# Optimization experiments

Hardware: AMD Instinct MI355X
Metric: run time of the kernel (lower is better)

## Reference

```python
import jax, jax.numpy as jnp
import numpy as np

NQ = 8          # n_qubits (attention and ffn)
DIM = 2 ** NQ   # state-vector dimension
EPS = 1e-5      # nn.LayerNorm default eps


def _layernorm(x, g, b):
    m = jnp.mean(x, axis=-1, keepdims=True)
    v = jnp.mean((x - m) ** 2, axis=-1, keepdims=True)
    return (x - m) * jax.lax.rsqrt(v + EPS) * g + b


def _attn_quantum(tok, theta):
    """Batched 8-qubit state-vector sim: RX(tok_i)+RX(theta_i) per wire, CNOT ring, <Z_i>.
    tok: [N, 8] -> returns [N, 8]."""
    N = tok.shape[0]
    half = 0.5 * (tok + theta)  # RX(a)RX(b) = RX(a+b) on same wire
    # per-wire amplitude RX(a)|0> = (cos(a/2), -i sin(a/2))
    re = jnp.stack([jnp.cos(half), jnp.zeros_like(half)], axis=-1)
    im = jnp.stack([jnp.zeros_like(half), -jnp.sin(half)], axis=-1)
    amp = jax.lax.complex(re, im)  # [N, 8, 2]
    # build product state with wire 0 as the leading qubit axis: [N, 2, ..., 2]
    state = amp[:, 0, :]
    for w in range(1, NQ):
        state = state[..., None] * amp[:, w, :].reshape((N,) + (1,) * w + (2,))
    # CNOT ring: (0,1),(1,2),...,(6,7),(7,0)
    pairs = [(i, i + 1) for i in range(NQ - 1)] + [(NQ - 1, 0)]
    for c, t in pairs:
        flipped = jnp.flip(state, axis=t + 1)
        mask = jnp.arange(2).reshape((1,) * (c + 1) + (2,) + (1,) * (NQ - 1 - c))
        state = jnp.where(mask == 1, flipped, state)
    probs = (state.real ** 2 + state.imag ** 2).reshape(N, DIM)
    # <Z_w> = sum_k probs[k] * (1 - 2*bit_w(k)); wire 0 is most significant bit
    bits = (jnp.arange(DIM)[None, :] >> (NQ - 1 - jnp.arange(NQ)[:, None])) & 1
    signs = (1.0 - 2.0 * bits).astype(probs.dtype)  # [8, 256]
    return probs @ signs.T


def _ffn_quantum(tok, phi):
    """Product state per wire: RY(phi_i) RX(tok_i) |0>, then <Z_i>. tok: [..., 8]."""
    ct, st = jnp.cos(0.5 * tok), jnp.sin(0.5 * tok)
    cp, sp = jnp.cos(0.5 * phi), jnp.sin(0.5 * phi)
    # v0 = cp*ct + i*sp*st ; v1 = sp*ct - i*cp*st ; z = |v0|^2 - |v1|^2
    return (cp * ct) ** 2 + (sp * st) ** 2 - (sp * ct) ** 2 - (cp * st) ** 2


def setup_inputs() -> dict:
    key = jax.random.key(0)
    ks = jax.random.split(key, 8)
    B, S, E, F = 32, 2048, 8, 2048
    x = jax.random.normal(ks[0], (B, S, E), dtype=jnp.float32)
    theta = jax.random.uniform(ks[1], (NQ,), dtype=jnp.float32, minval=-np.pi, maxval=np.pi)
    phi = jax.random.uniform(ks[2], (NQ,), dtype=jnp.float32, minval=-np.pi, maxval=np.pi)
    W1 = jax.random.normal(ks[3], (F, NQ), dtype=jnp.float32) / np.sqrt(NQ)
    b1 = jax.random.normal(ks[4], (F,), dtype=jnp.float32) * 0.01
    W2 = jax.random.normal(ks[5], (E, F), dtype=jnp.float32) / np.sqrt(F)
    b2 = jax.random.normal(ks[6], (E,), dtype=jnp.float32) * 0.01
    gamma1 = jnp.ones((E,), dtype=jnp.float32)
    beta1 = jnp.zeros((E,), dtype=jnp.float32)
    gamma2 = jnp.ones((E,), dtype=jnp.float32)
    beta2 = jnp.zeros((E,), dtype=jnp.float32)
    return {"x": x, "theta": theta, "phi": phi, "W1": W1, "b1": b1, "W2": W2,
            "b2": b2, "gamma1": gamma1, "beta1": beta1, "gamma2": gamma2, "beta2": beta2}


def reference(x, theta, phi, W1, b1, W2, b2, gamma1, beta1, gamma2, beta2):
    B, S, E = x.shape
    attn = _attn_quantum(x.reshape(B * S, E), theta).reshape(B, S, E)
    h = _layernorm(x + attn, gamma1, beta1)            # dropout is identity (eval)
    z = _ffn_quantum(h, phi)                            # [B, S, 8]
    f = jax.nn.relu(z @ W1.T + b1) @ W2.T + b2          # linear1 -> relu -> linear2
    return _layernorm(h + f, gamma2, beta2)
```

## Files before the change

### kernel.cpp

```cpp
#include <hip/hip_runtime.h>
#include <math.h>

#define NQ 8
#define FDIM 2048
#define EPSV 1e-5f

typedef __attribute__((ext_vector_type(8))) short short8v;
typedef __attribute__((ext_vector_type(16))) float f32x16;

__device__ __forceinline__ unsigned pk_bf16(float lo, float hi) {
    unsigned r;
    asm("v_cvt_pk_bf16_f32 %0, %1, %2" : "=v"(r) : "v"(lo), "v"(hi));
    return r;
}

__device__ __forceinline__ short8v pack4(unsigned a, unsigned b, unsigned c, unsigned d) {
    uint4 w; w.x = a; w.y = b; w.z = c; w.w = d;
    return __builtin_bit_cast(short8v, w);
}

#define MFMA32 __builtin_amdgcn_mfma_f32_32x32x16_bf16

#define RP(C, d0, d1)                                                   \
  { const f32x16 m_ = __builtin_elementwise_max(C, zeroC);              \
    d0 = pack4(pk_bf16(m_[0],  m_[1]),  pk_bf16(m_[2],  m_[3]),         \
               pk_bf16(m_[4],  m_[5]),  pk_bf16(m_[6],  m_[7]));        \
    d1 = pack4(pk_bf16(m_[8],  m_[9]),  pk_bf16(m_[10], m_[11]),        \
               pk_bf16(m_[12], m_[13]), pk_bf16(m_[14], m_[15])); }

#define ITER(AUSE, ALOAD, B0USE, B1USE, C2IDX)                          \
  {                                                                     \
    short8v p00, p01, p10, p11;                                         \
    RP(C1_0, p00, p01); RP(C1_1, p10, p11);                             \
    C1_0 = MFMA32(AUSE, b1S0, zeroC, 0, 0, 0);                          \
    C1_1 = MFMA32(AUSE, b1S1, zeroC, 0, 0, 0);                          \
    acc0 = MFMA32(p00, B0USE, acc0, 0, 0, 0);                           \
    acc1 = MFMA32(p10, B0USE, acc1, 0, 0, 0);                           \
    acc0 = MFMA32(p01, B1USE, acc0, 0, 0, 0);                           \
    acc1 = MFMA32(p11, B1USE, acc1, 0, 0, 0);                           \
    short8v p20, p21, p30, p31;                                         \
    RP(C1_2, p20, p21); RP(C1_3, p30, p31);                             \
    C1_2 = MFMA32(AUSE, b1S2, zeroC, 0, 0, 0);                          \
    C1_3 = MFMA32(AUSE, b1S3, zeroC, 0, 0, 0);                          \
    acc2 = MFMA32(p20, B0USE, acc2, 0, 0, 0);                           \
    acc3 = MFMA32(p30, B0USE, acc3, 0, 0, 0);                           \
    acc2 = MFMA32(p21, B1USE, acc2, 0, 0, 0);                           \
    acc3 = MFMA32(p31, B1USE, acc3, 0, 0, 0);                           \
    ALOAD = *reinterpret_cast<const short8v*>(W1p + (C2IDX) * 512);     \
    B0USE = *reinterpret_cast<const short8v*>(W2p + (C2IDX) * 32);      \
    B1USE = *reinterpret_cast<const short8v*>(W2p + (C2IDX) * 32 + 16); \
  }

__launch_bounds__(512, 2)
__global__ void qtb_kernel(const float* __restrict__ x,
                           const float* __restrict__ theta,
                           const float* __restrict__ phi,
                           const float* __restrict__ W1,
                           const float* __restrict__ b1,
                           const float* __restrict__ W2,
                           const float* __restrict__ b2,
                           const float* __restrict__ g1,
                           const float* __restrict__ be1,
                           const float* __restrict__ g2,
                           const float* __restrict__ be2,
                           float* __restrict__ out)
{
    __shared__ short W1f[64 * 512];
    __shared__ short W2s[8 * 2056];
    __shared__ float park[8][1024];
    __shared__ float hLds[256 * 8];

    const int tid  = threadIdx.x;
    const int lane = tid & 63;
    const int wid  = tid >> 6;
    const int g    = wid & 1;
    const int q    = wid >> 1;
    const int hi2  = lane >> 5;
    const int il   = lane & 31;
    const int tbase = blockIdx.x * 256 + g * 128;

    const float4 xA0 = reinterpret_cast<const float4*>(x + (size_t)(tbase + lane) * NQ)[0];
    const float4 xA1 = reinterpret_cast<const float4*>(x + (size_t)(tbase + lane) * NQ)[1];
    const float4 xB0 = reinterpret_cast<const float4*>(x + (size_t)(tbase + 64 + lane) * NQ)[0];
    const float4 xB1 = reinterpret_cast<const float4*>(x + (size_t)(tbase + 64 + lane) * NQ)[1];

    float4 w1lo[4], w1hi[4]; float bk4[4];
#pragma unroll
    for (int it = 0; it < 4; ++it) {
        const int k = tid + it * 512;
        w1lo[it] = *reinterpret_cast<const float4*>(W1 + (size_t)k * NQ);
        w1hi[it] = *reinterpret_cast<const float4*>(W1 + (size_t)k * NQ + 4);
        bk4[it]  = b1[k];
    }
    float4 w2v[8];
#pragma unroll
    for (int it = 0; it < 8; ++it) {
        const int idx = tid + it * 512;
        const int i = idx >> 9, kq = idx & 511;
        w2v[it] = *reinterpret_cast<const float4*>(W2 + (size_t)i * FDIM + kq * 4);
    }

    float h[2][8];
    unsigned zpkt[2][4];
#pragma unroll
    for (int tt = 0; tt < 2; ++tt) {
        const float4 x0 = tt ? xB0 : xA0;
        const float4 x1 = tt ? xB1 : xA1;
        const float xv[8] = {x0.x, x0.y, x0.z, x0.w, x1.x, x1.y, x1.z, x1.w};

        float c[8];
#pragma unroll
        for (int j = 0; j < 8; ++j) c[j] = __cosf(xv[j] + theta[j]);
        float attn[8];
        attn[0] = ((c[1] * c[2]) * (c[3] * c[4])) * ((c[5] * c[6]) * c[7]);
        {
            float p = c[0];
#pragma unroll
            for (int j = 1; j < 8; ++j) { p *= c[j]; attn[j] = p; }
        }
        float s[8];
#pragma unroll
        for (int j = 0; j < 8; ++j) s[j] = xv[j] + attn[j];
        float mean = 0.f;
#pragma unroll
        for (int j = 0; j < 8; ++j) mean += s[j];
        mean *= 0.125f;
        float var = 0.f;
#pragma unroll
        for (int j = 0; j < 8; ++j) { float d = s[j] - mean; var = fmaf(d, d, var); }
        var *= 0.125f;
        const float rs = rsqrtf(var + EPSV);
#pragma unroll
        for (int j = 0; j < 8; ++j) h[tt][j] = (s[j] - mean) * rs * g1[j] + be1[j];

        float zv[8];
#pragma unroll
        for (int j = 0; j < 8; ++j) zv[j] = __cosf(phi[j]) * __cosf(h[tt][j]);
#pragma unroll
        for (int p = 0; p < 4; ++p) zpkt[tt][p] = pk_bf16(zv[2 * p], zv[2 * p + 1]);
    }

    if (q == 0) {
        float4* hp0 = reinterpret_cast<float4*>(&hLds[(g * 128 + lane) * 8]);
        hp0[0] = make_float4(h[0][0], h[0][1], h[0][2], h[0][3]);
        hp0[1] = make_float4(h[0][4], h[0][5], h[0][6], h[0][7]);
        float4* hp1 = reinterpret_cast<float4*>(&hLds[(g * 128 + 64 + lane) * 8]);
        hp1[0] = make_float4(h[1][0], h[1][1], h[1][2], h[1][3]);
        hp1[1] = make_float4(h[1][4], h[1][5], h[1][6], h[1][7]);
    }

    unsigned zs[2][2][4];
#pragma unroll
    for (int tt = 0; tt < 2; ++tt)
#pragma unroll
        for (int p = 0; p < 4; ++p) {
            zs[tt][0][p] = (unsigned)__shfl((int)zpkt[tt][p], il);
            zs[tt][1][p] = (unsigned)__shfl((int)zpkt[tt][p], 32 + il);
        }
    const unsigned biasv = 0x00003f80u;
    const short8v b1S0 = pack4(hi2 ? zs[0][0][2] : zs[0][0][0],
                               hi2 ? zs[0][0][3] : zs[0][0][1],
                               hi2 ? 0u : biasv, 0u);
    const short8v b1S1 = pack4(hi2 ? zs[0][1][2] : zs[0][1][0],
                               hi2 ? zs[0][1][3] : zs[0][1][1],
                               hi2 ? 0u : biasv, 0u);
    const short8v b1S2 = pack4(hi2 ? zs[1][0][2] : zs[1][0][0],
                               hi2 ? zs[1][0][3] : zs[1][0][1],
                               hi2 ? 0u : biasv, 0u);
    const short8v b1S3 = pack4(hi2 ? zs[1][1][2] : zs[1][1][0],
                               hi2 ? zs[1][1][3] : zs[1][1][1],
                               hi2 ? 0u : biasv, 0u);

#pragma unroll
    for (int it = 0; it < 4; ++it) {
        const int k = tid + it * 512;
        uint4 d0, d1;
        d0.x = pk_bf16(w1lo[it].x, w1lo[it].y); d0.y = pk_bf16(w1lo[it].z, w1lo[it].w);
        d0.z = pk_bf16(bk4[it], 0.f);           d0.w = 0u;
        d1.x = pk_bf16(w1hi[it].x, w1hi[it].y); d1.y = pk_bf16(w1hi[it].z, w1hi[it].w);
        d1.z = 0u;                              d1.w = 0u;
        *reinterpret_cast<uint4*>(&W1f[(k >> 5) * 512 + (k & 31) * 8])        = d0;
        *reinterpret_cast<uint4*>(&W1f[(k >> 5) * 512 + ((k & 31) + 32) * 8]) = d1;
    }
#pragma unroll
    for (int it = 0; it < 8; ++it) {
        const int idx = tid + it * 512;
        const int i = idx >> 9, kq = idx & 511;
        const int k0 = kq * 4;
        const int quad = (k0 >> 2) & 3;
        const int posq = (0x3120 >> (quad * 4)) & 0xF;
        const int dcol = (k0 & ~15) | (posq * 4);
        uint2 pkw; pkw.x = pk_bf16(w2v[it].x, w2v[it].y); pkw.y = pk_bf16(w2v[it].z, w2v[it].w);
        *reinterpret_cast<uint2*>(&W2s[i * 2056 + dcol]) = pkw;
    }
    __syncthreads();

    f32x16 zeroC;
#pragma unroll
    for (int e = 0; e < 16; ++e) zeroC[e] = 0.f;
    f32x16 acc0 = zeroC, acc1 = zeroC, acc2 = zeroC, acc3 = zeroC;

    const int ir = il & 7;
    const short* W1p = &W1f[(q * 16) * 512 + lane * 8];
    const short* W2p = &W2s[ir * 2056 + (q * 16) * 32 + hi2 * 8];

    short8v A1a = *reinterpret_cast<const short8v*>(W1p);
    short8v B0a = *reinterpret_cast<const short8v*>(W2p);
    short8v B1a = *reinterpret_cast<const short8v*>(W2p + 16);
    f32x16 C1_0 = MFMA32(A1a, b1S0, zeroC, 0, 0, 0);
    f32x16 C1_1 = MFMA32(A1a, b1S1, zeroC, 0, 0, 0);
    f32x16 C1_2 = MFMA32(A1a, b1S2, zeroC, 0, 0, 0);
    f32x16 C1_3 = MFMA32(A1a, b1S3, zeroC, 0, 0, 0);
    short8v A1b = *reinterpret_cast<const short8v*>(W1p + 512);
    short8v B0b = *reinterpret_cast<const short8v*>(W2p + 32);
    short8v B1b = *reinterpret_cast<const short8v*>(W2p + 32 + 16);

#pragma unroll
    for (int t = 0; t < 16; t += 2) {
        ITER(A1b, A1a, B0a, B1a, (t + 2) & 15);
        ITER(A1a, A1b, B0b, B1b, (t + 3) & 15);
    }

    if (il < 8) {
        float* fb = &park[wid][0];
#pragma unroll
        for (int r = 0; r < 16; ++r) {
            const int trow = (r & 3) + 8 * (r >> 2) + 4 * hi2;
            fb[trow * 8 + il]         = acc0[r];
            fb[(32 + trow) * 8 + il]  = acc1[r];
            fb[(64 + trow) * 8 + il]  = acc2[r];
            fb[(96 + trow) * 8 + il]  = acc3[r];
        }
    }
    __syncthreads();

    if (q == 0) {
#pragma unroll
        for (int tt = 0; tt < 2; ++tt) {
            const int tloc = tt * 64 + lane;
            float fv[8] = {0.f, 0.f, 0.f, 0.f, 0.f, 0.f, 0.f, 0.f};
#pragma unroll
            for (int qq = 0; qq < 4; ++qq) {
                const float* pb = &park[qq * 2 + g][tloc * 8];
                const float4 f0 = *reinterpret_cast<const float4*>(pb);
                const float4 f1 = *reinterpret_cast<const float4*>(pb + 4);
                fv[0] += f0.x; fv[1] += f0.y; fv[2] += f0.z; fv[3] += f0.w;
                fv[4] += f1.x; fv[5] += f1.y; fv[6] += f1.z; fv[7] += f1.w;
            }

            const float4 h0 = reinterpret_cast<const float4*>(&hLds[(g * 128 + tloc) * 8])[0];
            const float4 h1 = reinterpret_cast<const float4*>(&hLds[(g * 128 + tloc) * 8])[1];
            const float hv[8] = {h0.x, h0.y, h0.z, h0.w, h1.x, h1.y, h1.z, h1.w};

            float y[8];
#pragma unroll
            for (int j = 0; j < 8; ++j) y[j] = hv[j] + fv[j] + b2[j];
            float mean2 = 0.f;
#pragma unroll
            for (int j = 0; j < 8; ++j) mean2 += y[j];
            mean2 *= 0.125f;
            float var2 = 0.f;
#pragma unroll
            for (int j = 0; j < 8; ++j) { float d = y[j] - mean2; var2 = fmaf(d, d, var2); }
            var2 *= 0.125f;
            const float rs2 = rsqrtf(var2 + EPSV);

            float o[8];
#pragma unroll
            for (int j = 0; j < 8; ++j) o[j] = (y[j] - mean2) * rs2 * g2[j] + be2[j];

            const int token = blockIdx.x * 256 + g * 128 + tloc;
            float4* op = reinterpret_cast<float4*>(out + (size_t)token * NQ);
            op[0] = make_float4(o[0], o[1], o[2], o[3]);
            op[1] = make_float4(o[4], o[5], o[6], o[7]);
        }
    }
}

extern "C" void kernel_launch(void* const* d_in, const int* in_sizes, int n_in,
                              void* d_out, int out_size, void* d_ws, size_t ws_size,
                              hipStream_t stream) {
    const float* x     = (const float*)d_in[0];
    const float* theta = (const float*)d_in[1];
    const float* phi   = (const float*)d_in[2];
    const float* W1    = (const float*)d_in[3];
    const float* b1    = (const float*)d_in[4];
    const float* W2    = (const float*)d_in[5];
    const float* b2    = (const float*)d_in[6];
    const float* g1    = (const float*)d_in[7];
    const float* be1   = (const float*)d_in[8];
    const float* g2    = (const float*)d_in[9];
    const float* be2   = (const float*)d_in[10];
    float* out = (float*)d_out;

    const int ntok = in_sizes[0] / NQ;
    const int grid = ntok / 256;

    qtb_kernel<<<grid, 512, 0, stream>>>(x, theta, phi, W1, b1, W2, b2,
                                         g1, be1, g2, be2, out);
}
```

Before: 20.56 us.

## Specialize warps: half compute token prologue, half stage weights into LDS

Before, all 8 waves redundantly computed attention, layernorm and z for their token group, and each also loaded a slice of W1/W2. Now waves 0-3 each compute one token per lane once, writing packed z and h to LDS. Waves 4-7 meanwhile load and convert all of W1 and W2 into LDS. The MFMA operands are then read from the zLds buffer instead of built with cross-lane shuffles, and the final layernorm is spread over four waves instead of two. This removes duplicated transcendental work and lets weight staging overlap the prologue, at the cost of more LDS and higher register use in the weight-loading waves.

```diff
diff --git a/kernel.cpp b/kernel.cpp
--- a/kernel.cpp
+++ b/kernel.cpp
@@ -67,8 +67,9 @@
 {
     __shared__ short W1f[64 * 512];
     __shared__ short W2s[8 * 2056];
-    __shared__ float park[8][1024];
+    __shared__ float parkF[8][1024];
     __shared__ float hLds[256 * 8];
+    __shared__ unsigned zLds[256][6];
 
     const int tid  = threadIdx.x;
     const int lane = tid & 63;
@@ -77,35 +78,12 @@
     const int q    = wid >> 1;
     const int hi2  = lane >> 5;
     const int il   = lane & 31;
-    const int tbase = blockIdx.x * 256 + g * 128;
-
-    const float4 xA0 = reinterpret_cast<const float4*>(x + (size_t)(tbase + lane) * NQ)[0];
-    const float4 xA1 = reinterpret_cast<const float4*>(x + (size_t)(tbase + lane) * NQ)[1];
-    const float4 xB0 = reinterpret_cast<const float4*>(x + (size_t)(tbase + 64 + lane) * NQ)[0];
-    const float4 xB1 = reinterpret_cast<const float4*>(x + (size_t)(tbase + 64 + lane) * NQ)[1];
-
-    float4 w1lo[4], w1hi[4]; float bk4[4];
-#pragma unroll
-    for (int it = 0; it < 4; ++it) {
-        const int k = tid + it * 512;
-        w1lo[it] = *reinterpret_cast<const float4*>(W1 + (size_t)k * NQ);
-        w1hi[it] = *reinterpret_cast<const float4*>(W1 + (size_t)k * NQ + 4);
-        bk4[it]  = b1[k];
-    }
-    float4 w2v[8];
-#pragma unroll
-    for (int it = 0; it < 8; ++it) {
-        const int idx = tid + it * 512;
-        const int i = idx >> 9, kq = idx & 511;
-        w2v[it] = *reinterpret_cast<const float4*>(W2 + (size_t)i * FDIM + kq * 4);
-    }
-
-    float h[2][8];
-    unsigned zpkt[2][4];
-#pragma unroll
-    for (int tt = 0; tt < 2; ++tt) {
-        const float4 x0 = tt ? xB0 : xA0;
-        const float4 x1 = tt ? xB1 : xA1;
+    const int tb   = blockIdx.x * 256;
+
+    if (wid < 4) {
+        const int tl = wid * 64 + lane;
+        const float4 x0 = reinterpret_cast<const float4*>(x + (size_t)(tb + tl) * NQ)[0];
+        const float4 x1 = reinterpret_cast<const float4*>(x + (size_t)(tb + tl) * NQ)[1];
         const float xv[8] = {x0.x, x0.y, x0.z, x0.w, x1.x, x1.y, x1.z, x1.w};
 
         float c[8];
@@ -130,70 +108,80 @@
         for (int j = 0; j < 8; ++j) { float d = s[j] - mean; var = fmaf(d, d, var); }
         var *= 0.125f;
         const float rs = rsqrtf(var + EPSV);
-#pragma unroll
-        for (int j = 0; j < 8; ++j) h[tt][j] = (s[j] - mean) * rs * g1[j] + be1[j];
+        float h[8];
+#pragma unroll
+        for (int j = 0; j < 8; ++j) h[j] = (s[j] - mean) * rs * g1[j] + be1[j];
 
         float zv[8];
 #pragma unroll
-        for (int j = 0; j < 8; ++j) zv[j] = __cosf(phi[j]) * __cosf(h[tt][j]);
-#pragma unroll
-        for (int p = 0; p < 4; ++p) zpkt[tt][p] = pk_bf16(zv[2 * p], zv[2 * p + 1]);
-    }
-
-    if (q == 0) {
-        float4* hp0 = reinterpret_cast<float4*>(&hLds[(g * 128 + lane) * 8]);
-        hp0[0] = make_float4(h[0][0], h[0][1], h[0][2], h[0][3]);
-        hp0[1] = make_float4(h[0][4], h[0][5], h[0][6], h[0][7]);
-        float4* hp1 = reinterpret_cast<float4*>(&hLds[(g * 128 + 64 + lane) * 8]);
-        hp1[0] = make_float4(h[1][0], h[1][1], h[1][2], h[1][3]);
-        hp1[1] = make_float4(h[1][4], h[1][5], h[1][6], h[1][7]);
-    }
-
-    unsigned zs[2][2][4];
-#pragma unroll
-    for (int tt = 0; tt < 2; ++tt)
-#pragma unroll
-        for (int p = 0; p < 4; ++p) {
-            zs[tt][0][p] = (unsigned)__shfl((int)zpkt[tt][p], il);
-            zs[tt][1][p] = (unsigned)__shfl((int)zpkt[tt][p], 32 + il);
-        }
+        for (int j = 0; j < 8; ++j) zv[j] = __cosf(phi[j]) * __cosf(h[j]);
+
+        uint2 zlo, zhi;
+        zlo.x = pk_bf16(zv[0], zv[1]); zlo.y = pk_bf16(zv[2], zv[3]);
+        zhi.x = pk_bf16(zv[4], zv[5]); zhi.y = pk_bf16(zv[6], zv[7]);
+        *reinterpret_cast<uint2*>(&zLds[tl][0]) = zlo;
+        *reinterpret_cast<uint2*>(&zLds[tl][2]) = zhi;
+
+        float4* hp = reinterpret_cast<float4*>(&hLds[tl * 8]);
+        hp[0] = make_float4(h[0], h[1], h[2], h[3]);
+        hp[1] = make_float4(h[4], h[5], h[6], h[7]);
+    } else {
+        const int t2 = tid - 256;
+        {
+            float4 wa[8], wb[8]; float bb[8];
+#pragma unroll
+            for (int it = 0; it < 8; ++it) {
+                const int k = t2 + it * 256;
+                wa[it] = *reinterpret_cast<const float4*>(W1 + (size_t)k * NQ);
+                wb[it] = *reinterpret_cast<const float4*>(W1 + (size_t)k * NQ + 4);
+                bb[it] = b1[k];
+            }
+#pragma unroll
+            for (int it = 0; it < 8; ++it) {
+                const int k = t2 + it * 256;
+                uint4 d0, d1;
+                d0.x = pk_bf16(wa[it].x, wa[it].y); d0.y = pk_bf16(wa[it].z, wa[it].w);
+                d0.z = pk_bf16(bb[it], 0.f);        d0.w = 0u;
+                d1.x = pk_bf16(wb[it].x, wb[it].y); d1.y = pk_bf16(wb[it].z, wb[it].w);
+                d1.z = 0u;                          d1.w = 0u;
+                *reinterpret_cast<uint4*>(&W1f[(k >> 5) * 512 + (k & 31) * 8])        = d0;
+                *reinterpret_cast<uint4*>(&W1f[(k >> 5) * 512 + ((k & 31) + 32) * 8]) = d1;
+            }
+        }
+#pragma unroll
+        for (int bt = 0; bt < 2; ++bt) {
+            float4 w[8];
+#pragma unroll
+            for (int it = 0; it < 8; ++it) {
+                const int idx = t2 + (bt * 8 + it) * 256;
+                const int i = idx >> 9, kq = idx & 511;
+                w[it] = *reinterpret_cast<const float4*>(W2 + (size_t)i * FDIM + kq * 4);
+            }
+#pragma unroll
+            for (int it = 0; it < 8; ++it) {
+                const int idx = t2 + (bt * 8 + it) * 256;
+                const int i = idx >> 9, kq = idx & 511;
+                const int k0 = kq * 4;
+                const int quad = (k0 >> 2) & 3;
+                const int posq = (0x3120 >> (quad * 4)) & 0xF;
+                const int dcol = (k0 & ~15) | (posq * 4);
+                uint2 pkw; pkw.x = pk_bf16(w[it].x, w[it].y); pkw.y = pk_bf16(w[it].z, w[it].w);
+                *reinterpret_cast<uint2*>(&W2s[i * 2056 + dcol]) = pkw;
+            }
+        }
+    }
+    __syncthreads();
+
     const unsigned biasv = 0x00003f80u;
-    const short8v b1S0 = pack4(hi2 ? zs[0][0][2] : zs[0][0][0],
-                               hi2 ? zs[0][0][3] : zs[0][0][1],
-                               hi2 ? 0u : biasv, 0u);
-    const short8v b1S1 = pack4(hi2 ? zs[0][1][2] : zs[0][1][0],
-                               hi2 ? zs[0][1][3] : zs[0][1][1],
-                               hi2 ? 0u : biasv, 0u);
-    const short8v b1S2 = pack4(hi2 ? zs[1][0][2] : zs[1][0][0],
-                               hi2 ? zs[1][0][3] : zs[1][0][1],
-                               hi2 ? 0u : biasv, 0u);
-    const short8v b1S3 = pack4(hi2 ? zs[1][1][2] : zs[1][1][0],
-                               hi2 ? zs[1][1][3] : zs[1][1][1],
-                               hi2 ? 0u : biasv, 0u);
-
-#pragma unroll
-    for (int it = 0; it < 4; ++it) {
-        const int k = tid + it * 512;
-        uint4 d0, d1;
-        d0.x = pk_bf16(w1lo[it].x, w1lo[it].y); d0.y = pk_bf16(w1lo[it].z, w1lo[it].w);
-        d0.z = pk_bf16(bk4[it], 0.f);           d0.w = 0u;
-        d1.x = pk_bf16(w1hi[it].x, w1hi[it].y); d1.y = pk_bf16(w1hi[it].z, w1hi[it].w);
-        d1.z = 0u;                              d1.w = 0u;
-        *reinterpret_cast<uint4*>(&W1f[(k >> 5) * 512 + (k & 31) * 8])        = d0;
-        *reinterpret_cast<uint4*>(&W1f[(k >> 5) * 512 + ((k & 31) + 32) * 8]) = d1;
-    }
-#pragma unroll
-    for (int it = 0; it < 8; ++it) {
-        const int idx = tid + it * 512;
-        const int i = idx >> 9, kq = idx & 511;
-        const int k0 = kq * 4;
-        const int quad = (k0 >> 2) & 3;
-        const int posq = (0x3120 >> (quad * 4)) & 0xF;
-        const int dcol = (k0 & ~15) | (posq * 4);
-        uint2 pkw; pkw.x = pk_bf16(w2v[it].x, w2v[it].y); pkw.y = pk_bf16(w2v[it].z, w2v[it].w);
-        *reinterpret_cast<uint2*>(&W2s[i * 2056 + dcol]) = pkw;
-    }
-    __syncthreads();
+    const int zcol = hi2 * 2;
+    const uint2 z0 = *reinterpret_cast<const uint2*>(&zLds[g * 128 +      il][zcol]);
+    const uint2 z1 = *reinterpret_cast<const uint2*>(&zLds[g * 128 + 32 + il][zcol]);
+    const uint2 z2 = *reinterpret_cast<const uint2*>(&zLds[g * 128 + 64 + il][zcol]);
+    const uint2 z3 = *reinterpret_cast<const uint2*>(&zLds[g * 128 + 96 + il][zcol]);
+    const short8v b1S0 = pack4(z0.x, z0.y, hi2 ? 0u : biasv, 0u);
+    const short8v b1S1 = pack4(z1.x, z1.y, hi2 ? 0u : biasv, 0u);
+    const short8v b1S2 = pack4(z2.x, z2.y, hi2 ? 0u : biasv, 0u);
+    const short8v b1S3 = pack4(z3.x, z3.y, hi2 ? 0u : biasv, 0u);
 
     f32x16 zeroC;
 #pragma unroll
@@ -222,7 +210,7 @@
     }
 
     if (il < 8) {
-        float* fb = &park[wid][0];
+        float* fb = &parkF[wid][0];
 #pragma unroll
         for (int r = 0; r < 16; ++r) {
             const int trow = (r & 3) + 8 * (r >> 2) + 4 * hi2;
@@ -234,46 +222,44 @@
     }
     __syncthreads();
 
-    if (q == 0) {
-#pragma unroll
-        for (int tt = 0; tt < 2; ++tt) {
-            const int tloc = tt * 64 + lane;
-            float fv[8] = {0.f, 0.f, 0.f, 0.f, 0.f, 0.f, 0.f, 0.f};
-#pragma unroll
-            for (int qq = 0; qq < 4; ++qq) {
-                const float* pb = &park[qq * 2 + g][tloc * 8];
-                const float4 f0 = *reinterpret_cast<const float4*>(pb);
-                const float4 f1 = *reinterpret_cast<const float4*>(pb + 4);
-                fv[0] += f0.x; fv[1] += f0.y; fv[2] += f0.z; fv[3] += f0.w;
-                fv[4] += f1.x; fv[5] += f1.y; fv[6] += f1.z; fv[7] += f1.w;
-            }
-
-            const float4 h0 = reinterpret_cast<const float4*>(&hLds[(g * 128 + tloc) * 8])[0];
-            const float4 h1 = reinterpret_cast<const float4*>(&hLds[(g * 128 + tloc) * 8])[1];
-            const float hv[8] = {h0.x, h0.y, h0.z, h0.w, h1.x, h1.y, h1.z, h1.w};
-
-            float y[8];
-#pragma unroll
-            for (int j = 0; j < 8; ++j) y[j] = hv[j] + fv[j] + b2[j];
-            float mean2 = 0.f;
-#pragma unroll
-            for (int j = 0; j < 8; ++j) mean2 += y[j];
-            mean2 *= 0.125f;
-            float var2 = 0.f;
-#pragma unroll
-            for (int j = 0; j < 8; ++j) { float d = y[j] - mean2; var2 = fmaf(d, d, var2); }
-            var2 *= 0.125f;
-            const float rs2 = rsqrtf(var2 + EPSV);
-
-            float o[8];
-#pragma unroll
-            for (int j = 0; j < 8; ++j) o[j] = (y[j] - mean2) * rs2 * g2[j] + be2[j];
-
-            const int token = blockIdx.x * 256 + g * 128 + tloc;
-            float4* op = reinterpret_cast<float4*>(out + (size_t)token * NQ);
-            op[0] = make_float4(o[0], o[1], o[2], o[3]);
-            op[1] = make_float4(o[4], o[5], o[6], o[7]);
-        }
+    if (wid < 4) {
+        const int tl   = wid * 64 + lane;
+        const int ge   = tl >> 7;
+        const int tloc = tl & 127;
+        float fv[8] = {0.f, 0.f, 0.f, 0.f, 0.f, 0.f, 0.f, 0.f};
+#pragma unroll
+        for (int qq = 0; qq < 4; ++qq) {
+            const float* pb = &parkF[qq * 2 + ge][tloc * 8];
+            const float4 f0 = *reinterpret_cast<const float4*>(pb);
+            const float4 f1 = *reinterpret_cast<const float4*>(pb + 4);
+            fv[0] += f0.x; fv[1] += f0.y; fv[2] += f0.z; fv[3] += f0.w;
+            fv[4] += f1.x; fv[5] += f1.y; fv[6] += f1.z; fv[7] += f1.w;
+        }
+
+        const float4 h0 = reinterpret_cast<const float4*>(&hLds[tl * 8])[0];
+        const float4 h1 = reinterpret_cast<const float4*>(&hLds[tl * 8])[1];
+        const float hv[8] = {h0.x, h0.y, h0.z, h0.w, h1.x, h1.y, h1.z, h1.w};
+
+        float y[8];
+#pragma unroll
+        for (int j = 0; j < 8; ++j) y[j] = hv[j] + fv[j] + b2[j];
+        float mean2 = 0.f;
+#pragma unroll
+        for (int j = 0; j < 8; ++j) mean2 += y[j];
+        mean2 *= 0.125f;
+        float var2 = 0.f;
+#pragma unroll
+        for (int j = 0; j < 8; ++j) { float d = y[j] - mean2; var2 = fmaf(d, d, var2); }
+        var2 *= 0.125f;
+        const float rs2 = rsqrtf(var2 + EPSV);
+
+        float o[8];
+#pragma unroll
+        for (int j = 0; j < 8; ++j) o[j] = (y[j] - mean2) * rs2 * g2[j] + be2[j];
+
+        float4* op = reinterpret_cast<float4*>(out + (size_t)(tb + tl) * NQ);
+        op[0] = make_float4(o[0], o[1], o[2], o[3]);
+        op[1] = make_float4(o[4], o[5], o[6], o[7]);
     }
 }
 
```

Result: no change. 20.21 us (-1.7%).
